# Kernel optimization log

Measured on AMD Instinct MI355X. Metric: run time of the kernel, lower is better.

## Reference

```python
import jax, jax.numpy as jnp
import numpy as np

WS = 8          # window size
NUM_HEADS = 12


def setup_inputs() -> dict:
    key = jax.random.key(0)
    k1, k2, k3 = jax.random.split(key, 3)
    B, N, C = 16, 4096, 384
    x = jax.random.normal(k1, (B, N, C), dtype=jnp.float32)
    # torch Linear weights stored as [in, out] so forward is x @ W
    qkv_w = jax.random.normal(k2, (C, 3 * C), dtype=jnp.float32) * (C ** -0.5)
    proj_w = jax.random.normal(k3, (C, C), dtype=jnp.float32) * (C ** -0.5)
    proj_b = jnp.zeros((C,), dtype=jnp.float32)
    return {"x": x, "qkv_w": qkv_w, "proj_w": proj_w, "proj_b": proj_b}


def reference(x, qkv_w, proj_w, proj_b):
    B, N, C = x.shape
    H = W = int(np.sqrt(N))
    hg, wg = H // WS, W // WS
    G = hg * wg
    nh = NUM_HEADS
    hd = C // nh
    scale = hd ** -0.5

    # window partition: [B, N, C] -> [B, hg, wg, ws, ws, C]
    xw = x.reshape(B, hg, WS, wg, WS, C).transpose(0, 1, 3, 2, 4, 5)
    xw = xw.reshape(B, G, WS * WS, C)

    # qkv projection -> [3, B, G, nh, ws*ws, hd]
    qkv = (xw @ qkv_w).reshape(B, G, WS * WS, 3, nh, hd)
    qkv = qkv.transpose(3, 0, 1, 4, 2, 5)
    q, k, v = qkv[0], qkv[1], qkv[2]

    attn = jnp.einsum('bgnqd,bgnkd->bgnqk', q, k) * scale
    attn = jax.nn.softmax(attn, axis=-1)
    out = jnp.einsum('bgnqk,bgnkd->bgnqd', attn, v)

    # merge heads and reverse window partition
    out = out.transpose(0, 1, 3, 2, 4).reshape(B, hg, wg, WS, WS, C)
    out = out.transpose(0, 1, 3, 2, 4, 5).reshape(B, N, C)

    return out @ proj_w + proj_b
```

## Files before the change

kernel.cpp:

```cpp
#include <hip/hip_runtime.h>
#include <stdint.h>

typedef unsigned short ushort_t;
typedef __bf16 bf16x8 __attribute__((ext_vector_type(8)));
typedef float floatx4 __attribute__((ext_vector_type(4)));
typedef float floatx16 __attribute__((ext_vector_type(16)));
typedef unsigned short ushort8 __attribute__((ext_vector_type(8)));

__device__ __forceinline__ ushort_t f2b(float f) {
  union { float f; unsigned u; } v; v.f = f;
  unsigned r = v.u + 0x7fffu + ((v.u >> 16) & 1u);
  return (ushort_t)(r >> 16);
}
__device__ __forceinline__ ushort_t b2u(float f) {
  union { __bf16 b; ushort_t u; } v; v.b = (__bf16)f; return v.u;
}
__device__ __forceinline__ bf16x8 cvt8(const float* p) {
  floatx4 f0 = *(const floatx4*)p;
  floatx4 f1 = *(const floatx4*)(p + 4);
  union { bf16x8 v; __bf16 e[8]; } u;
#pragma unroll
  for (int j = 0; j < 4; ++j) u.e[j] = (__bf16)f0[j];
#pragma unroll
  for (int j = 0; j < 4; ++j) u.e[4 + j] = (__bf16)f1[j];
  return u.v;
}

__device__ __forceinline__ unsigned cvtpk(float a, float b) {
  unsigned r;
  asm("v_cvt_pk_bf16_f32 %0, %1, %2" : "=v"(r) : "v"(a), "v"(b));
  return r;
}
__device__ __forceinline__ void plswap(unsigned& x, unsigned& y) {
  asm("v_permlane32_swap_b32 %0, %1" : "+v"(x), "+v"(y));
}

__device__ __forceinline__ void async16(const ushort_t* g, ushort_t* l) {
  __builtin_amdgcn_global_load_lds(
      (const __attribute__((address_space(1))) void*)g,
      (__attribute__((address_space(3))) void*)l, 16, 0, 0);
}

__global__ __launch_bounds__(256) void cvt_x(const float* __restrict__ src,
                                             ushort_t* __restrict__ dst, int n8) {
  int i = blockIdx.x * 256 + threadIdx.x;
  if (i < n8) *(bf16x8*)&dst[(size_t)i * 8] = cvt8(src + (size_t)i * 8);
}

__global__ void transpose_k(const float* __restrict__ src,
                            ushort_t* __restrict__ dst, int R, int Cc) {
  int idx = blockIdx.x * 256 + threadIdx.x;
  if (idx < R * Cc) {
    int r = idx / Cc, c = idx % Cc;
    dst[(size_t)c * R + r] = f2b(src[idx]);
  }
}

template <int C_F32>
__global__ __launch_bounds__(256) void gemm_bt(
    const ushort_t* __restrict__ A, int lda,
    const ushort_t* __restrict__ Bt,
    const float* __restrict__ bias, void* __restrict__ C_,
    int M, int N, int K) {
  __shared__ __align__(16) ushort_t As[128 * 64];
  __shared__ __align__(16) ushort_t Bs[128 * 64];
  const int t = threadIdx.x;
  const int nwg = gridDim.x;
  const int per = nwg >> 3;
  const int swz = (blockIdx.x & 7) * per + (blockIdx.x >> 3);
  const int ntn = N >> 7;
  const int m0 = (swz / ntn) << 7;
  const int n0 = (swz % ntn) << 7;
  const int w = t >> 6, lane = t & 63;
  const int wy = (w >> 1) << 6;
  const int wx = (w & 1) << 6;
  const int l15 = lane & 15;
  const int quad = lane >> 4;
  const int quad4 = quad << 2;
  floatx4 acc[4][4] = {};
  const int srow = t >> 3;
  const int sc = (((t & 7) ^ (srow & 7)) << 3);
  const ushort_t* gA = A + (size_t)(m0 + srow) * lda + sc;
  const ushort_t* gB = Bt + (size_t)(n0 + srow) * K + sc;
  for (int k0 = 0; k0 < K; k0 += 64) {
    __syncthreads();
#pragma unroll
    for (int r4 = 0; r4 < 4; ++r4) {
      async16(gA + (size_t)r4 * 32 * lda + k0, &As[r4 * 2048 + t * 8]);
      async16(gB + (size_t)r4 * 32 * K + k0, &Bs[r4 * 2048 + t * 8]);
    }
    __syncthreads();
#pragma unroll
    for (int kk = 0; kk < 2; ++kk) {
      bf16x8 af[4], bfr[4];
#pragma unroll
      for (int i = 0; i < 4; ++i) {
        int row = wy + i * 16 + l15;
        af[i] = *(const bf16x8*)&As[row * 64 + ((((kk << 2) | quad) ^ (row & 7)) << 3)];
      }
#pragma unroll
      for (int j = 0; j < 4; ++j) {
        int row = wx + j * 16 + l15;
        bfr[j] = *(const bf16x8*)&Bs[row * 64 + ((((kk << 2) | quad) ^ (row & 7)) << 3)];
      }
#pragma unroll
      for (int i = 0; i < 4; ++i)
#pragma unroll
        for (int j = 0; j < 4; ++j)
          acc[i][j] = __builtin_amdgcn_mfma_f32_16x16x32_bf16(
              af[i], bfr[j], acc[i][j], 0, 0, 0);
    }
  }
  float bv[4] = {0.f, 0.f, 0.f, 0.f};
  if (bias != nullptr) {
#pragma unroll
    for (int j = 0; j < 4; ++j) bv[j] = bias[n0 + wx + j * 16 + l15];
  }
#pragma unroll
  for (int i = 0; i < 4; ++i) {
#pragma unroll
    for (int r = 0; r < 4; ++r) {
      size_t row = (size_t)(m0 + wy + i * 16 + quad4 + r);
      if (C_F32) {
        float* cp = (float*)C_ + row * N + (n0 + wx + l15);
#pragma unroll
        for (int j = 0; j < 4; ++j) cp[j * 16] = acc[i][j][r] + bv[j];
      } else {
        ushort_t* cp = (ushort_t*)C_ + row * N + (n0 + wx + l15);
#pragma unroll
        for (int j = 0; j < 4; ++j) cp[j * 16] = f2b(acc[i][j][r] + bv[j]);
      }
    }
  }
}

__global__ __launch_bounds__(256, 2) void win_attn(
    const ushort_t* __restrict__ QKV, ushort_t* __restrict__ O, int ostride) {
  __shared__ __align__(16) ushort_t Vt[4][32 * 72];
  const int blk = blockIdx.x;
  const int b = blk >> 6, g = blk & 63;
  const int gy = g >> 3, gx = g & 7;
  const int t = threadIdx.x, w = t >> 6, lane = t & 63;
  const int l31 = lane & 31, bh = lane >> 5;
  const size_t bbase = (size_t)b * 4096 + (size_t)(gy * 8) * 64 + gx * 8;
  const float scale = 0.17677669529663687f;

  for (int hi = 0; hi < 3; ++hi) {
    const int h = w * 3 + hi;
    const size_t hq = (size_t)h * 32;

    {
      size_t row = bbase + (size_t)(lane >> 3) * 64 + (lane & 7);
      const ushort_t* vp = QKV + row * 1152 + 768 + hq;
#pragma unroll
      for (int i = 0; i < 4; ++i) {
        ushort8 vv = *(const ushort8*)(vp + i * 8);
#pragma unroll
        for (int j = 0; j < 8; ++j) Vt[w][(i * 8 + j) * 72 + lane] = vv[j];
      }
    }

    bf16x8 qf[2][2];
#pragma unroll
    for (int qt = 0; qt < 2; ++qt) {
      int tok = qt * 32 + l31;
      size_t row = bbase + (size_t)(tok >> 3) * 64 + (tok & 7);
#pragma unroll
      for (int dc = 0; dc < 2; ++dc)
        qf[qt][dc] = *(const bf16x8*)(QKV + row * 1152 + hq + dc * 16 + bh * 8);
    }

    floatx16 st[2][2] = {};
#pragma unroll
    for (int kt = 0; kt < 2; ++kt) {
      bf16x8 kf[2];
      int tok = kt * 32 + l31;
      size_t row = bbase + (size_t)(tok >> 3) * 64 + (tok & 7);
#pragma unroll
      for (int dc = 0; dc < 2; ++dc)
        kf[dc] = *(const bf16x8*)(QKV + row * 1152 + 384 + hq + dc * 16 + bh * 8);
#pragma unroll
      for (int qt = 0; qt < 2; ++qt)
#pragma unroll
        for (int dc = 0; dc < 2; ++dc)
          st[kt][qt] = __builtin_amdgcn_mfma_f32_32x32x16_bf16(
              kf[dc], qf[qt][dc], st[kt][qt], 0, 0, 0);
    }

    float rs[2] = {0.f, 0.f};
#pragma unroll
    for (int kt = 0; kt < 2; ++kt)
#pragma unroll
      for (int qt = 0; qt < 2; ++qt)
#pragma unroll
        for (int r = 0; r < 16; ++r) {
          float e = __expf(st[kt][qt][r] * scale);
          st[kt][qt][r] = e;
          rs[qt] += e;
        }
#pragma unroll
    for (int qt = 0; qt < 2; ++qt) rs[qt] += __shfl_xor(rs[qt], 32);
    float inv[2] = {1.0f / rs[0], 1.0f / rs[1]};

    floatx16 o[2] = {};
#pragma unroll
    for (int s = 0; s < 4; ++s) {
      const int kt = s >> 1, r1x = (s & 1) << 1;
      bf16x8 vf = *(const bf16x8*)&Vt[w][l31 * 72 + s * 16 + bh * 8];
#pragma unroll
      for (int qt = 0; qt < 2; ++qt) {
        float iv = inv[qt];
        unsigned x0 = cvtpk(st[kt][qt][4 * r1x + 0] * iv, st[kt][qt][4 * r1x + 1] * iv);
        unsigned x1 = cvtpk(st[kt][qt][4 * r1x + 2] * iv, st[kt][qt][4 * r1x + 3] * iv);
        unsigned y0 = cvtpk(st[kt][qt][4 * r1x + 4] * iv, st[kt][qt][4 * r1x + 5] * iv);
        unsigned y1 = cvtpk(st[kt][qt][4 * r1x + 6] * iv, st[kt][qt][4 * r1x + 7] * iv);
        plswap(x0, y0);
        plswap(x1, y1);
        union { unsigned d[4]; bf16x8 v; } pa;
        pa.d[0] = x0; pa.d[1] = x1; pa.d[2] = y0; pa.d[3] = y1;
        o[qt] = __builtin_amdgcn_mfma_f32_32x32x16_bf16(pa.v, vf, o[qt], 0, 0, 0);
      }
    }

#pragma unroll
    for (int qt = 0; qt < 2; ++qt)
#pragma unroll
      for (int r = 0; r < 16; ++r) {
        int tok = qt * 32 + (r & 3) + 8 * (r >> 2) + 4 * bh;
        size_t row = bbase + (size_t)(tok >> 3) * 64 + (tok & 7);
        O[row * (size_t)ostride + hq + l31] = b2u(o[qt][r]);
      }
  }
}

extern "C" void kernel_launch(void* const* d_in, const int* in_sizes, int n_in,
                              void* d_out, int out_size, void* d_ws, size_t ws_size,
                              hipStream_t stream) {
  const float* x      = (const float*)d_in[0];
  const float* qkv_w  = (const float*)d_in[1];
  const float* proj_w = (const float*)d_in[2];
  const float* proj_b = (const float*)d_in[3];
  float* out = (float*)d_out;

  const int M = 16 * 4096;
  const size_t need =
      ((size_t)M * 1152 + (size_t)M * 384 + 1152 * 384 + 384 * 384) * 2;
  if (ws_size < need) return;

  ushort_t* qkv    = (ushort_t*)d_ws;
  ushort_t* xb     = qkv + (size_t)M * 1152;
  ushort_t* qkvwT  = xb + (size_t)M * 384;
  ushort_t* projwT = qkvwT + (size_t)1152 * 384;

  cvt_x<<<(M * 384 / 8 + 255) / 256, 256, 0, stream>>>(x, xb, M * 384 / 8);
  transpose_k<<<(384 * 1152 + 255) / 256, 256, 0, stream>>>(qkv_w, qkvwT, 384, 1152);
  transpose_k<<<(384 * 384 + 255) / 256, 256, 0, stream>>>(proj_w, projwT, 384, 384);

  gemm_bt<0><<<(M / 128) * (1152 / 128), 256, 0, stream>>>(
      xb, 384, qkvwT, nullptr, qkv, M, 1152, 384);

  win_attn<<<16 * 64, 256, 0, stream>>>(qkv, qkv, 1152);

  gemm_bt<1><<<(M / 128) * (384 / 128), 256, 0, stream>>>(
      qkv, 1152, projwT, proj_b, out, M, 384, 384);
}
```

Baseline: 342.1 us.

## Fuse output projection into window attention kernel via LDS-staged attention output

Each window's attention output is now kept in a swizzled 48KB shared-memory tile instead of being written back into the QKV buffer. The same block then runs the 64x384x384 projection GEMM with MFMA, adds the bias and writes fp32 output directly. This removes one kernel launch and the global round trip of the attention output. In exchange, the larger shared-memory footprint may lower occupancy, and the projection weights are read from global memory with no LDS reuse in every block.

```diff
diff --git a/kernel.cpp b/kernel.cpp
--- a/kernel.cpp
+++ b/kernel.cpp
@@ -134,14 +134,17 @@
   }
 }
 
-__global__ __launch_bounds__(256, 2) void win_attn(
-    const ushort_t* __restrict__ QKV, ushort_t* __restrict__ O, int ostride) {
+__global__ __launch_bounds__(256, 2) void attn_proj(
+    const ushort_t* __restrict__ QKV, const ushort_t* __restrict__ Bt,
+    const float* __restrict__ bias, float* __restrict__ out) {
   __shared__ __align__(16) ushort_t Vt[4][32 * 72];
+  __shared__ __align__(16) ushort_t Ao[64 * 384];
   const int blk = blockIdx.x;
   const int b = blk >> 6, g = blk & 63;
   const int gy = g >> 3, gx = g & 7;
   const int t = threadIdx.x, w = t >> 6, lane = t & 63;
   const int l31 = lane & 31, bh = lane >> 5;
+  const int l15 = lane & 15, quad = lane >> 4, quad4 = quad << 2;
   const size_t bbase = (size_t)b * 4096 + (size_t)(gy * 8) * 64 + gx * 8;
   const float scale = 0.17677669529663687f;
 
@@ -222,14 +225,57 @@
       }
     }
 
+    const int base64 = (h >> 1) << 6;
+    const int cbase = ((h & 1) << 2) | (l31 >> 3);
+    const int e7 = l31 & 7;
 #pragma unroll
     for (int qt = 0; qt < 2; ++qt)
 #pragma unroll
       for (int r = 0; r < 16; ++r) {
         int tok = qt * 32 + (r & 3) + 8 * (r >> 2) + 4 * bh;
-        size_t row = bbase + (size_t)(tok >> 3) * 64 + (tok & 7);
-        O[row * (size_t)ostride + hq + l31] = b2u(o[qt][r]);
-      }
+        int c = cbase ^ (tok & 7);
+        Ao[tok * 384 + base64 + (c << 3) + e7] = b2u(o[qt][r]);
+      }
+  }
+
+  __syncthreads();
+
+  floatx4 acc[4][6] = {};
+  for (int ks = 0; ks < 12; ++ks) {
+    bf16x8 af[4];
+#pragma unroll
+    for (int i = 0; i < 4; ++i) {
+      int row = i * 16 + l15;
+      int c = (((ks & 1) << 2) | quad) ^ (row & 7);
+      af[i] = *(const bf16x8*)&Ao[row * 384 + ((ks >> 1) << 6) + (c << 3)];
+    }
+    bf16x8 bfr[6];
+#pragma unroll
+    for (int j = 0; j < 6; ++j) {
+      int n = w * 96 + j * 16 + l15;
+      bfr[j] = *(const bf16x8*)&Bt[(size_t)n * 384 + ks * 32 + (quad << 3)];
+    }
+#pragma unroll
+    for (int i = 0; i < 4; ++i)
+#pragma unroll
+      for (int j = 0; j < 6; ++j)
+        acc[i][j] = __builtin_amdgcn_mfma_f32_16x16x32_bf16(
+            af[i], bfr[j], acc[i][j], 0, 0, 0);
+  }
+
+  float bv[6];
+#pragma unroll
+  for (int j = 0; j < 6; ++j) bv[j] = bias[w * 96 + j * 16 + l15];
+#pragma unroll
+  for (int i = 0; i < 4; ++i) {
+#pragma unroll
+    for (int r = 0; r < 4; ++r) {
+      int tok = i * 16 + quad4 + r;
+      size_t grow = bbase + (size_t)(tok >> 3) * 64 + (tok & 7);
+      float* cp = out + grow * 384 + w * 96 + l15;
+#pragma unroll
+      for (int j = 0; j < 6; ++j) cp[j * 16] = acc[i][j][r] + bv[j];
+    }
   }
 }
 
@@ -259,8 +305,5 @@
   gemm_bt<0><<<(M / 128) * (1152 / 128), 256, 0, stream>>>(
       xb, 384, qkvwT, nullptr, qkv, M, 1152, 384);
 
-  win_attn<<<16 * 64, 256, 0, stream>>>(qkv, qkv, 1152);
-
-  gemm_bt<1><<<(M / 128) * (384 / 128), 256, 0, stream>>>(
-      qkv, 1152, projwT, proj_b, out, M, 384, 384);
-}
+  attn_proj<<<16 * 64, 256, 0, stream>>>(qkv, projwT, proj_b, out);
+}
```

Measured after the change: 329.6 us. 1.04x faster.
